# Performance work log

Hardware: AMD Instinct MI355X
Metric: run time of the kernel (lower is better)

The kernel has to match this reference:

```python
import jax, jax.numpy as jnp
import numpy as np

NUM_CLUSTERS = 5000  # labels.max()+1, fixed statically for jit
B, K, D, N = 256, 64, 2048, 50000
NHID, H2, NCLASS = 512, 256, 2


def setup_inputs() -> dict:
    key = jax.random.key(0)
    ks = jax.random.split(key, 16)
    s = lambda f_in: 1.0 / np.sqrt(f_in)
    return {
        "indexes": jax.random.randint(ks[0], (B,), 0, N),
        "features": jax.random.normal(ks[1], (N, D), dtype=jnp.float32),
        "labels": jax.random.randint(ks[2], (N,), 0, NUM_CLUSTERS),
        "domain": 1,
        "ori_0": 0,
        "ori_knn_neighbor": jax.random.randint(ks[3], (B, K), 0, N),
        "all_pred": jax.random.normal(ks[4], (B, K, NCLASS), dtype=jnp.float32),
        # GraphConv params (L-GCN style: weight [2*in, out])
        "W1": jax.random.normal(ks[5], (2 * D, NHID), jnp.float32) * s(2 * D),
        "b1": jnp.zeros((NHID,), jnp.float32),
        "W2": jax.random.normal(ks[6], (2 * NHID, H2), jnp.float32) * s(2 * NHID),
        "b2": jnp.zeros((H2,), jnp.float32),
        # classifier: Linear(256,256) -> PReLU(256) -> Linear(256,2)
        "Wc1": jax.random.normal(ks[7], (H2, H2), jnp.float32) * s(H2),
        "bc1": jnp.zeros((H2,), jnp.float32),
        "prelu_a": jnp.full((H2,), 0.25, jnp.float32),
        "Wc2": jax.random.normal(ks[8], (H2, NCLASS), jnp.float32) * s(H2),
        "bc2": jnp.zeros((NCLASS,), jnp.float32),
    }


def _gconv(x, A, W, b):
    # MeanAggregator: bmm(A, x); GraphConv: relu(cat([x, Ax]) @ W + b)
    agg = jnp.einsum('bkj,bjd->bkd', A, x)
    cat = jnp.concatenate([x, agg], axis=-1)
    return jax.nn.relu(jnp.einsum('bkd,df->bkf', cat, W) + b)


def reference(indexes, features, labels, domain, ori_0, ori_knn_neighbor, all_pred,
              W1, b1, W2, b2, Wc1, bc1, prelu_a, Wc2, bc2):
    # ---- cluster mean features (torch: index_add_ then divide; no_grad) ----
    clu_sum = jax.ops.segment_sum(features, labels, num_segments=NUM_CLUSTERS)
    nums = jax.ops.segment_sum(jnp.ones((features.shape[0],), features.dtype),
                               labels, num_segments=NUM_CLUSTERS)
    clu_mean = clu_sum / jnp.maximum(nums, 1.0)[:, None]  # [C, D]

    # ---- batched per-query subgraph construction (vectorized over B) ----
    clu_lab = labels[ori_knn_neighbor]            # [B, K]
    clu_feat = clu_mean[clu_lab]                  # [B, K, D]
    clu_feat = clu_feat.at[:, 0, :].set(features[indexes])  # pivot = raw feature

    A = jnp.einsum('bkd,bjd->bkj', clu_feat, clu_feat)       # pairwise similarity
    A = A * jnp.exp(all_pred[:, :, 1])[:, None, :]           # confidence weighting
    A = jax.nn.softmax(A, axis=-1)                           # row-normalized adjacency

    x = clu_feat / jnp.linalg.norm(clu_feat, axis=-1, keepdims=True)
    x = x - x[:, 0:1, :]                                     # center on pivot

    # (entire construction above is under torch.no_grad)
    x = jax.lax.stop_gradient(x)
    A = jax.lax.stop_gradient(A)

    # ---- GCN layers + classifier ----
    x = _gconv(x, A, W1, b1)      # [B, K, 512]
    x = _gconv(x, A, W2, b2)      # [B, K, 256]
    x0 = x.reshape(-1, H2)        # [B*K, 256]
    h = x0 @ Wc1 + bc1
    h = jnp.where(h >= 0, h, prelu_a * h)  # PReLU(256)
    logits = h @ Wc2 + bc2                 # [B*K, 2]

    # output_feat=True branch
    simm = jnp.sum(clu_mean * clu_mean, axis=1)                   # [C]
    pred = jax.nn.softmax(logits.reshape(B, K, NCLASS), axis=2)   # [B, K, 2]
    return (pred, simm)
```

## Files before the change

kernel.cpp:

```cpp
#include <hip/hip_runtime.h>
#include <math.h>

#define Bq 256
#define Kn 64
#define Dd 2048
#define Nn 50000
#define Cc 5000
#define NHID 512
#define H2d 256
#define LDH 264
#define MP 5376
#define PIVROW 5120

typedef __attribute__((ext_vector_type(8))) __bf16 bf16x8;
typedef __attribute__((ext_vector_type(4))) float f32x4;

__device__ __forceinline__ unsigned short f2bf(float f) {
    union { float f; unsigned int u; } v;
    v.f = f;
    unsigned int u = v.u;
    unsigned int r = (u + 0x7fff + ((u >> 16) & 1)) >> 16;
    return (unsigned short)r;
}
__device__ __forceinline__ float bf2f(unsigned short h) {
    union { unsigned int u; float f; } v;
    v.u = ((unsigned int)h) << 16;
    return v.f;
}


__global__ void k_zero_int(int* __restrict__ p, int n) {
    int i = blockIdx.x * 256 + threadIdx.x;
    if (i < n) p[i] = 0;
}

__global__ void k_count(const int* __restrict__ labels, int* __restrict__ cnt, int n) {
    int i = blockIdx.x * 256 + threadIdx.x;
    if (i < n) atomicAdd(&cnt[labels[i]], 1);
}

__global__ __launch_bounds__(1024) void k_scan(const int* __restrict__ cnt,
                                               int* __restrict__ off,
                                               int* __restrict__ pos, int C) {
    __shared__ int s[1024];
    __shared__ int carry;
    int tid = threadIdx.x;
    if (tid == 0) carry = 0;
    __syncthreads();
    for (int base = 0; base < C; base += 1024) {
        int i = base + tid;
        int v = (i < C) ? cnt[i] : 0;
        s[tid] = v;
        __syncthreads();
        for (int o = 1; o < 1024; o <<= 1) {
            int t = (tid >= o) ? s[tid - o] : 0;
            __syncthreads();
            s[tid] += t;
            __syncthreads();
        }
        int excl = carry + s[tid] - v;
        if (i < C) { off[i] = excl; pos[i] = excl; }
        __syncthreads();
        if (tid == 0) carry += s[1023];
        __syncthreads();
    }
}

__global__ void k_scatter(const int* __restrict__ labels, int* __restrict__ pos,
                          int* __restrict__ rowidx, int n) {
    int i = blockIdx.x * 256 + threadIdx.x;
    if (i < n) {
        int p = atomicAdd(&pos[labels[i]], 1);
        rowidx[p] = i;
    }
}

__global__ __launch_bounds__(256) void k_meansimm(
    const float* __restrict__ feat, const int* __restrict__ rowidx,
    const int* __restrict__ off, const int* __restrict__ cnt,
    float* __restrict__ clu_mean, float* __restrict__ simm,
    unsigned short* __restrict__ cn) {
    int c = blockIdx.x;
    int t = threadIdx.x;
    int n = cnt[c], st = off[c];
    float4 a0 = {0.f, 0.f, 0.f, 0.f}, a1 = {0.f, 0.f, 0.f, 0.f};
    for (int r = 0; r < n; r++) {
        const float* row = feat + (size_t)rowidx[st + r] * Dd;
        float4 v0 = *(const float4*)(row + t * 4);
        float4 v1 = *(const float4*)(row + 1024 + t * 4);
        a0.x += v0.x; a0.y += v0.y; a0.z += v0.z; a0.w += v0.w;
        a1.x += v1.x; a1.y += v1.y; a1.z += v1.z; a1.w += v1.w;
    }
    float sc = 1.f / (float)(n > 1 ? n : 1);
    a0.x *= sc; a0.y *= sc; a0.z *= sc; a0.w *= sc;
    a1.x *= sc; a1.y *= sc; a1.z *= sc; a1.w *= sc;
    float* outr = clu_mean + (size_t)c * Dd;
    *(float4*)(outr + t * 4) = a0;
    *(float4*)(outr + 1024 + t * 4) = a1;
    float ss = a0.x * a0.x + a0.y * a0.y + a0.z * a0.z + a0.w * a0.w +
               a1.x * a1.x + a1.y * a1.y + a1.z * a1.z + a1.w * a1.w;
    __shared__ float red[256];
    red[t] = ss;
    __syncthreads();
    for (int s2 = 128; s2 > 0; s2 >>= 1) {
        if (t < s2) red[t] += red[t + s2];
        __syncthreads();
    }
    if (t == 0) simm[c] = red[0];
    float tot = red[0];
    float rnn = (tot > 0.f) ? rsqrtf(tot) : 0.f;
    ushort4 c0, c1;
    c0.x = f2bf(a0.x * rnn); c0.y = f2bf(a0.y * rnn);
    c0.z = f2bf(a0.z * rnn); c0.w = f2bf(a0.w * rnn);
    c1.x = f2bf(a1.x * rnn); c1.y = f2bf(a1.y * rnn);
    c1.z = f2bf(a1.z * rnn); c1.w = f2bf(a1.w * rnn);
    unsigned short* cr = cn + (size_t)c * Dd;
    *(ushort4*)(cr + t * 4) = c0;
    *(ushort4*)(cr + 1024 + t * 4) = c1;
}

__global__ __launch_bounds__(256) void k_pivots(
    const float* __restrict__ feat, const int* __restrict__ indexes,
    unsigned short* __restrict__ PA) {
    int b = blockIdx.x, t = threadIdx.x;
    const float* row = feat + (size_t)indexes[b] * Dd;
    float4 v0 = *(const float4*)(row + t * 4);
    float4 v1 = *(const float4*)(row + 1024 + t * 4);
    float ss = v0.x * v0.x + v0.y * v0.y + v0.z * v0.z + v0.w * v0.w +
               v1.x * v1.x + v1.y * v1.y + v1.z * v1.z + v1.w * v1.w;
    __shared__ float red[256];
    red[t] = ss;
    __syncthreads();
    for (int s2 = 128; s2 > 0; s2 >>= 1) {
        if (t < s2) red[t] += red[t + s2];
        __syncthreads();
    }
    float tot = red[0];
    float rnn = (tot > 0.f) ? rsqrtf(tot) : 0.f;
    ushort4 c0, c1;
    c0.x = f2bf(v0.x * rnn); c0.y = f2bf(v0.y * rnn);
    c0.z = f2bf(v0.z * rnn); c0.w = f2bf(v0.w * rnn);
    c1.x = f2bf(v1.x * rnn); c1.y = f2bf(v1.y * rnn);
    c1.z = f2bf(v1.z * rnn); c1.w = f2bf(v1.w * rnn);
    unsigned short* cr = PA + (size_t)(PIVROW + b) * Dd;
    *(ushort4*)(cr + t * 4) = c0;
    *(ushort4*)(cr + 1024 + t * 4) = c1;
}

__global__ __launch_bounds__(256) void k_build_ax(
    const float* __restrict__ feat, const float* __restrict__ clu_mean,
    const int* __restrict__ labels, const int* __restrict__ indexes,
    const int* __restrict__ knn, const float* __restrict__ all_pred,
    float* __restrict__ Abuf) {
    __shared__ unsigned short Hs[64 * LDH];
    __shared__ unsigned short Ls[64 * LDH];
    __shared__ float Gs[64 * 65];
    __shared__ const float* rowp[64];
    __shared__ float wj64[64];

    int b = blockIdx.x, tid = threadIdx.x;
    int wave = tid >> 6, lane = tid & 63, quad = lane >> 4, l16 = lane & 15;

    if (tid < 64) {
        const float* p = (tid == 0) ? feat + (size_t)indexes[b] * Dd
                                    : clu_mean + (size_t)labels[knn[b * 64 + tid]] * Dd;
        rowp[tid] = p;
        wj64[tid] = expf(all_pred[(b * 64 + tid) * 2 + 1]);
    }
    __syncthreads();

    f32x4 acc[4];
#pragma unroll
    for (int j = 0; j < 4; j++) acc[j] = (f32x4){0.f, 0.f, 0.f, 0.f};

    for (int ch = 0; ch < 8; ch++) {
        int d0 = ch * 256;
        __syncthreads();
#pragma unroll
        for (int q = 0; q < 16; q++) {
            int e4 = tid + q * 256;
            int row = e4 >> 6;
            int c4 = (e4 & 63) * 4;
            float4 v = *(const float4*)(rowp[row] + d0 + c4);
            ushort4 h, l;
            h.x = f2bf(v.x); l.x = f2bf(v.x - bf2f(h.x));
            h.y = f2bf(v.y); l.y = f2bf(v.y - bf2f(h.y));
            h.z = f2bf(v.z); l.z = f2bf(v.z - bf2f(h.z));
            h.w = f2bf(v.w); l.w = f2bf(v.w - bf2f(h.w));
            *(ushort4*)&Hs[row * LDH + c4] = h;
            *(ushort4*)&Ls[row * LDH + c4] = l;
        }
        __syncthreads();
#pragma unroll
        for (int ks = 0; ks < 8; ks++) {
            int kk = ks * 32 + quad * 8;
            bf16x8 ah = *(const bf16x8*)&Hs[(wave * 16 + l16) * LDH + kk];
            bf16x8 al = *(const bf16x8*)&Ls[(wave * 16 + l16) * LDH + kk];
#pragma unroll
            for (int j = 0; j < 4; j++) {
                bf16x8 bh = *(const bf16x8*)&Hs[(j * 16 + l16) * LDH + kk];
                bf16x8 bl = *(const bf16x8*)&Ls[(j * 16 + l16) * LDH + kk];
                acc[j] = __builtin_amdgcn_mfma_f32_16x16x32_bf16(ah, bh, acc[j], 0, 0, 0);
                acc[j] = __builtin_amdgcn_mfma_f32_16x16x32_bf16(ah, bl, acc[j], 0, 0, 0);
                acc[j] = __builtin_amdgcn_mfma_f32_16x16x32_bf16(al, bh, acc[j], 0, 0, 0);
            }
        }
    }
    __syncthreads();
#pragma unroll
    for (int j = 0; j < 4; j++)
#pragma unroll
        for (int r = 0; r < 4; r++)
            Gs[(wave * 16 + quad * 4 + r) * 65 + j * 16 + l16] = acc[j][r];
    __syncthreads();
    if (tid < 64) {
        int r = tid;
        float mx = -1e30f;
        for (int c = 0; c < 64; c++) {
            float v = Gs[r * 65 + c] * wj64[c];
            mx = fmaxf(mx, v);
        }
        float s = 0.f;
        for (int c = 0; c < 64; c++) {
            float e = expf(Gs[r * 65 + c] * wj64[c] - mx);
            Gs[r * 65 + c] = e;
            s += e;
        }
        float inv = 1.f / s;
        float* Arow = Abuf + ((size_t)b * 64 + r) * 64;
        for (int c = 0; c < 64; c++) Arow[c] = Gs[r * 65 + c] * inv;
    }
}

template <int SPLIT>
__global__ __launch_bounds__(256) void k_pack_w(const float* __restrict__ W,
                                                unsigned short* __restrict__ Bp,
                                                int K, int Nhalf) {
    int Ntot = SPLIT ? 2 * Nhalf : Nhalf;
    int idx = blockIdx.x * 256 + threadIdx.x;
    int kb = idx / Ntot;
    int n = idx - kb * Ntot;
    ushort4 lo, hi;
    float v[8];
#pragma unroll
    for (int j = 0; j < 8; j++) {
        int k = kb * 8 + j;
        if (SPLIT)
            v[j] = (n < Nhalf) ? W[(size_t)k * Nhalf + n]
                               : W[(size_t)(K + k) * Nhalf + (n - Nhalf)];
        else
            v[j] = W[(size_t)k * Nhalf + n];
    }
    lo.x = f2bf(v[0]); lo.y = f2bf(v[1]); lo.z = f2bf(v[2]); lo.w = f2bf(v[3]);
    hi.x = f2bf(v[4]); hi.y = f2bf(v[5]); hi.z = f2bf(v[6]); hi.w = f2bf(v[7]);
    *(ushort4*)&Bp[(size_t)idx * 8] = lo;
    *(ushort4*)&Bp[(size_t)idx * 8 + 4] = hi;
}

template <int EPI>
__global__ __launch_bounds__(256) void gemm_bf16_mfma(
    const unsigned short* __restrict__ A, const unsigned short* __restrict__ Bp,
    float* __restrict__ C, int M, int K, int N,
    const float* __restrict__ bias, const float* __restrict__ pre_a) {
    __shared__ unsigned short Asm[128 * 32];
    __shared__ unsigned short Bsm[4 * 128 * 8];
    int tid = threadIdx.x;
    int wave = tid >> 6, lane = tid & 63;
    int quad = lane >> 4, l16 = lane & 15;
    int m0 = blockIdx.y * 128, n0 = blockIdx.x * 128;
    int wm = (wave >> 1) * 64, wn = (wave & 1) * 64;

    f32x4 acc[4][4];
#pragma unroll
    for (int i = 0; i < 4; i++)
#pragma unroll
        for (int j = 0; j < 4; j++) acc[i][j] = (f32x4){0.f, 0.f, 0.f, 0.f};

    int ia0 = wave * 2, ia1 = wave * 2 + 1;
    const unsigned short* gA0 = A + (size_t)(m0 + ia0 * 16 + (lane >> 2)) * K + (lane & 3) * 8;
    const unsigned short* gA1 = gA0 + (size_t)16 * K;
    const unsigned short* gB0 = Bp + (size_t)(n0 + lane) * 8 + (size_t)wave * N * 8;

    for (int k0 = 0; k0 < K; k0 += 32) {
        __syncthreads();
        size_t bko = (size_t)(k0 >> 3) * N * 8;
        __builtin_amdgcn_global_load_lds(
            (const __attribute__((address_space(1))) void*)(gA0 + k0),
            (__attribute__((address_space(3))) void*)(Asm + ia0 * 512), 16, 0, 0);
        __builtin_amdgcn_global_load_lds(
            (const __attribute__((address_space(1))) void*)(gA1 + k0),
            (__attribute__((address_space(3))) void*)(Asm + ia1 * 512), 16, 0, 0);
        __builtin_amdgcn_global_load_lds(
            (const __attribute__((address_space(1))) void*)(gB0 + bko),
            (__attribute__((address_space(3))) void*)(Bsm + wave * 1024), 16, 0, 0);
        __builtin_amdgcn_global_load_lds(
            (const __attribute__((address_space(1))) void*)(gB0 + bko + 512),
            (__attribute__((address_space(3))) void*)(Bsm + wave * 1024 + 512), 16, 0, 0);
        __syncthreads();

        bf16x8 a[4], b[4];
#pragma unroll
        for (int i = 0; i < 4; i++)
            a[i] = *(const bf16x8*)&Asm[(wm + i * 16 + l16) * 32 + quad * 8];
#pragma unroll
        for (int j = 0; j < 4; j++)
            b[j] = *(const bf16x8*)&Bsm[quad * 1024 + (wn + j * 16 + l16) * 8];
#pragma unroll
        for (int i = 0; i < 4; i++)
#pragma unroll
            for (int j = 0; j < 4; j++)
                acc[i][j] = __builtin_amdgcn_mfma_f32_16x16x32_bf16(
                    a[i], b[j], acc[i][j], 0, 0, 0);
    }

#pragma unroll
    for (int i = 0; i < 4; i++) {
#pragma unroll
        for (int j = 0; j < 4; j++) {
            int col = n0 + wn + j * 16 + l16;
            float bcol = (EPI == 1) ? bias[col] : 0.f;
            float acol = (EPI == 1) ? pre_a[col] : 0.f;
#pragma unroll
            for (int r = 0; r < 4; r++) {
                int row = m0 + wm + i * 16 + quad * 4 + r;
                float v = acc[i][j][r];
                if (EPI == 1) {
                    v += bcol;
                    v = (v >= 0.f) ? v : acol * v;
                }
                C[(size_t)row * N + col] = v;
            }
        }
    }
}

__global__ __launch_bounds__(256) void k_layer_agg1(
    const float* __restrict__ P, const float* __restrict__ Abuf,
    const int* __restrict__ labels, const int* __restrict__ knn,
    const float* __restrict__ bias, unsigned short* __restrict__ outp) {
    int b = blockIdx.x;
    int tid = threadIdx.x;
    __shared__ float Ast[64 * 68];
    __shared__ float Us[64 * 68];
    __shared__ int rowid[64];
    int ty = tid >> 4, tx = tid & 15;
    if (tid < 64)
        rowid[tid] = (tid == 0) ? (PIVROW + b) : labels[knn[b * 64 + tid]];
    const float* Ab = Abuf + (size_t)b * 64 * 64;
    for (int e4 = tid; e4 < 1024; e4 += 256) {
        float4 v = *(const float4*)(Ab + e4 * 4);
        int row = e4 >> 4;
        int c4 = (e4 & 15) * 4;
        Ast[(c4 + 0) * 68 + row] = v.x;
        Ast[(c4 + 1) * 68 + row] = v.y;
        Ast[(c4 + 2) * 68 + row] = v.z;
        Ast[(c4 + 3) * 68 + row] = v.w;
    }
    const float* Q = P + (size_t)(PIVROW + b) * 1024;
    for (int n0 = 0; n0 < NHID; n0 += 64) {
        __syncthreads();
#pragma unroll
        for (int kq = 0; kq < 4; kq++) {
            int e4 = tid + kq * 256;
            int row = e4 >> 4;
            int c4 = (e4 & 15) * 4;
            float4 v = *(const float4*)(P + (size_t)rowid[row] * 1024 + NHID + n0 + c4);
            float4 q = *(const float4*)(Q + NHID + n0 + c4);
            v.x -= q.x; v.y -= q.y; v.z -= q.z; v.w -= q.w;
            *(float4*)&Us[row * 68 + c4] = v;
        }
        __syncthreads();
        float acc[4][4];
#pragma unroll
        for (int i = 0; i < 4; i++)
#pragma unroll
            for (int j = 0; j < 4; j++) acc[i][j] = 0.f;
        for (int kk = 0; kk < 64; kk++) {
            float4 a4 = *(const float4*)&Ast[kk * 68 + ty * 4];
            float4 b4 = *(const float4*)&Us[kk * 68 + tx * 4];
            float aa[4] = {a4.x, a4.y, a4.z, a4.w};
            float bb[4] = {b4.x, b4.y, b4.z, b4.w};
#pragma unroll
            for (int i = 0; i < 4; i++)
#pragma unroll
                for (int j = 0; j < 4; j++) acc[i][j] += aa[i] * bb[j];
        }
#pragma unroll
        for (int i = 0; i < 4; i++) {
            int krow = ty * 4 + i;
            int m = b * 64 + krow;
            int n = n0 + tx * 4;
            float4 ua = *(const float4*)(P + (size_t)rowid[krow] * 1024 + n);
            float4 qa = *(const float4*)(Q + n);
            float v0 = fmaxf(ua.x - qa.x + acc[i][0] + bias[n + 0], 0.f);
            float v1 = fmaxf(ua.y - qa.y + acc[i][1] + bias[n + 1], 0.f);
            float v2 = fmaxf(ua.z - qa.z + acc[i][2] + bias[n + 2], 0.f);
            float v3 = fmaxf(ua.w - qa.w + acc[i][3] + bias[n + 3], 0.f);
            ushort4 o_;
            o_.x = f2bf(v0); o_.y = f2bf(v1); o_.z = f2bf(v2); o_.w = f2bf(v3);
            *(ushort4*)(outp + (size_t)m * NHID + n) = o_;
        }
        __syncthreads();
    }
}

template <int OBF>
__global__ __launch_bounds__(256) void k_layer_agg(
    const float* __restrict__ Uab, const float* __restrict__ Abuf,
    const float* __restrict__ bias, void* __restrict__ outp, int Nc) {
    int b = blockIdx.x;
    int tid = threadIdx.x;
    __shared__ float Ast[64 * 68];
    __shared__ float Us[64 * 68];
    int ty = tid >> 4, tx = tid & 15;
    const float* Ab = Abuf + (size_t)b * 64 * 64;
    for (int e4 = tid; e4 < 1024; e4 += 256) {
        float4 v = *(const float4*)(Ab + e4 * 4);
        int row = e4 >> 4;
        int c4 = (e4 & 15) * 4;
        Ast[(c4 + 0) * 68 + row] = v.x;
        Ast[(c4 + 1) * 68 + row] = v.y;
        Ast[(c4 + 2) * 68 + row] = v.z;
        Ast[(c4 + 3) * 68 + row] = v.w;
    }
    int ldU = 2 * Nc;
    const float* Ua = Uab;
    const float* Ub = Uab + Nc;
    for (int n0 = 0; n0 < Nc; n0 += 64) {
        __syncthreads();
#pragma unroll
        for (int kq = 0; kq < 4; kq++) {
            int e4 = tid + kq * 256;
            int row = e4 >> 4;
            int c4 = (e4 & 15) * 4;
            float4 v = *(const float4*)(Ub + (size_t)(b * 64 + row) * ldU + n0 + c4);
            *(float4*)&Us[row * 68 + c4] = v;
        }
        __syncthreads();
        float acc[4][4];
#pragma unroll
        for (int i = 0; i < 4; i++)
#pragma unroll
            for (int j = 0; j < 4; j++) acc[i][j] = 0.f;
        for (int kk = 0; kk < 64; kk++) {
            float4 a4 = *(const float4*)&Ast[kk * 68 + ty * 4];
            float4 b4 = *(const float4*)&Us[kk * 68 + tx * 4];
            float aa[4] = {a4.x, a4.y, a4.z, a4.w};
            float bb[4] = {b4.x, b4.y, b4.z, b4.w};
#pragma unroll
            for (int i = 0; i < 4; i++)
#pragma unroll
                for (int j = 0; j < 4; j++) acc[i][j] += aa[i] * bb[j];
        }
#pragma unroll
        for (int i = 0; i < 4; i++) {
            int m = b * 64 + ty * 4 + i;
            int n = n0 + tx * 4;
            float4 ua = *(const float4*)(Ua + (size_t)m * ldU + n);
            float v0 = fmaxf(ua.x + acc[i][0] + bias[n + 0], 0.f);
            float v1 = fmaxf(ua.y + acc[i][1] + bias[n + 1], 0.f);
            float v2 = fmaxf(ua.z + acc[i][2] + bias[n + 2], 0.f);
            float v3 = fmaxf(ua.w + acc[i][3] + bias[n + 3], 0.f);
            if (OBF) {
                ushort4 o_;
                o_.x = f2bf(v0); o_.y = f2bf(v1); o_.z = f2bf(v2); o_.w = f2bf(v3);
                *(ushort4*)((unsigned short*)outp + (size_t)m * Nc + n) = o_;
            } else {
                float4 o_ = {v0, v1, v2, v3};
                *(float4*)((float*)outp + (size_t)m * Nc + n) = o_;
            }
        }
        __syncthreads();
    }
}

__global__ __launch_bounds__(256) void k_logits(
    const float* __restrict__ h, const float* __restrict__ Wc2,
    const float* __restrict__ bc2, float* __restrict__ pred) {
    __shared__ float p0[256], p1[256];
    int tid = threadIdx.x;
    int r = tid >> 2, s = tid & 3;
    int m = blockIdx.x * 64 + r;
    const float* hr = h + (size_t)m * 256;
    float l0 = 0.f, l1 = 0.f;
    for (int k = s; k < 256; k += 4) {
        float hv = hr[k];
        l0 += hv * Wc2[2 * k];
        l1 += hv * Wc2[2 * k + 1];
    }
    p0[tid] = l0;
    p1[tid] = l1;
    __syncthreads();
    if (s == 0) {
        float L0 = p0[tid] + p0[tid + 1] + p0[tid + 2] + p0[tid + 3] + bc2[0];
        float L1 = p1[tid] + p1[tid + 1] + p1[tid + 2] + p1[tid + 3] + bc2[1];
        float mx = fmaxf(L0, L1);
        float e0 = expf(L0 - mx), e1 = expf(L1 - mx);
        float inv = 1.f / (e0 + e1);
        pred[2 * m] = e0 * inv;
        pred[2 * m + 1] = e1 * inv;
    }
}

extern "C" void kernel_launch(void* const* d_in, const int* in_sizes, int n_in,
                              void* d_out, int out_size, void* d_ws, size_t ws_size,
                              hipStream_t stream) {
    const int* indexes = (const int*)d_in[0];
    const float* features = (const float*)d_in[1];
    const int* labels = (const int*)d_in[2];
    const int* knn = (const int*)d_in[5];
    const float* all_pred = (const float*)d_in[6];
    const float* W1 = (const float*)d_in[7];
    const float* b1 = (const float*)d_in[8];
    const float* W2 = (const float*)d_in[9];
    const float* b2 = (const float*)d_in[10];
    const float* Wc1 = (const float*)d_in[11];
    const float* bc1 = (const float*)d_in[12];
    const float* pre_a = (const float*)d_in[13];
    const float* Wc2 = (const float*)d_in[14];
    const float* bc2 = (const float*)d_in[15];
    float* out = (float*)d_out;

    char* w = (char*)d_ws;
    size_t o = 0;
    auto carve = [&](size_t bytes) -> char* {
        char* p = w + o;
        o += (bytes + 255) & ~(size_t)255;
        return p;
    };
    int* cnt = (int*)carve((size_t)Cc * 4);
    int* off = (int*)carve((size_t)Cc * 4);
    int* pos = (int*)carve((size_t)Cc * 4);
    int* rowidx = (int*)carve((size_t)Nn * 4);
    float* clu_mean = (float*)carve((size_t)Cc * Dd * 4);
    unsigned short* PA = (unsigned short*)carve((size_t)MP * Dd * 2);
    float* Pout = (float*)carve((size_t)MP * 2 * NHID * 4);
    float* Abuf = (float*)carve((size_t)Bq * Kn * Kn * 4);
    unsigned short* Bp1 = (unsigned short*)carve((size_t)(Dd / 8) * 1024 * 8 * 2);
    unsigned short* x1 = (unsigned short*)carve((size_t)Bq * Kn * NHID * 2);
    float* V = (float*)carve((size_t)Bq * Kn * 2 * H2d * 4);
    unsigned short* Bp2 = (unsigned short*)carve((size_t)(NHID / 8) * 512 * 8 * 2);
    unsigned short* x2 = (unsigned short*)carve((size_t)Bq * Kn * H2d * 2);
    float* h = (float*)carve((size_t)Bq * Kn * H2d * 4);
    unsigned short* Bpc = (unsigned short*)carve((size_t)(H2d / 8) * 256 * 8 * 2);

    float* simm_out = out + (size_t)Bq * Kn * 2;

    k_zero_int<<<(Cc + 255) / 256, 256, 0, stream>>>(cnt, Cc);
    k_count<<<(Nn + 255) / 256, 256, 0, stream>>>(labels, cnt, Nn);
    k_scan<<<1, 1024, 0, stream>>>(cnt, off, pos, Cc);
    k_scatter<<<(Nn + 255) / 256, 256, 0, stream>>>(labels, pos, rowidx, Nn);

    {
        int npad = (PIVROW - Cc) * Dd / 2;
        k_zero_int<<<(npad + 255) / 256, 256, 0, stream>>>(
            (int*)(PA + (size_t)Cc * Dd), npad);
    }

    k_meansimm<<<Cc, 256, 0, stream>>>(features, rowidx, off, cnt, clu_mean,
                                       simm_out, PA);

    k_pivots<<<Bq, 256, 0, stream>>>(features, indexes, PA);

    k_build_ax<<<Bq, 256, 0, stream>>>(features, clu_mean, labels, indexes, knn,
                                       all_pred, Abuf);

    k_pack_w<1><<<(Dd / 8) * 1024 / 256, 256, 0, stream>>>(W1, Bp1, Dd, NHID);
    k_pack_w<1><<<(NHID / 8) * 512 / 256, 256, 0, stream>>>(W2, Bp2, NHID, H2d);
    k_pack_w<0><<<(H2d / 8) * 256 / 256, 256, 0, stream>>>(Wc1, Bpc, H2d, H2d);

    {
        dim3 g(1024 / 128, MP / 128);
        gemm_bf16_mfma<0><<<g, 256, 0, stream>>>(PA, Bp1, Pout, MP, Dd, 1024,
                                                 nullptr, nullptr);
    }
    k_layer_agg1<<<Bq, 256, 0, stream>>>(Pout, Abuf, labels, knn, b1, x1);

    {
        dim3 g(512 / 128, (Bq * Kn) / 128);
        gemm_bf16_mfma<0><<<g, 256, 0, stream>>>(x1, Bp2, V, Bq * Kn, NHID, 512,
                                                 nullptr, nullptr);
    }
    k_layer_agg<1><<<Bq, 256, 0, stream>>>(V, Abuf, b2, x2, H2d);

    {
        dim3 g(256 / 128, (Bq * Kn) / 128);
        gemm_bf16_mfma<1><<<g, 256, 0, stream>>>(x2, Bpc, h, Bq * Kn, H2d, 256,
                                                 bc1, pre_a);
    }
    k_logits<<<(Bq * Kn) / 64, 256, 0, stream>>>(h, Wc2, bc2, out);

    (void)in_sizes; (void)n_in; (void)out_size; (void)ws_size;
}
```

Measured before the change: 837.4 us.

## Fuse launches, premix layer-2 aggregation before GEMM, fold classifier into GEMM epilogue

Merges the zeroing, pivot normalisation and weight-packing kernels into fewer launches, and replaces the single-block scan with an atomic offset allocator. Layer 2 now aggregates x1 with A before the GEMM (A·x then one K=1024 GEMM with a bias+ReLU epilogue) instead of computing a 2x-wide output and aggregating after it. The classifier's second linear layer is folded into the first GEMM's epilogue through shuffle reductions and atomics, which removes the fp32 h buffer. Layer-1 aggregation is split across two blocks per query. The atomic allocator makes cluster order nondeterministic, and float atomics make the logit sums order-dependent.

```diff
diff --git a/kernel.cpp b/kernel.cpp
--- a/kernel.cpp
+++ b/kernel.cpp
@@ -28,10 +28,18 @@
     return v.f;
 }
 
-
-__global__ void k_zero_int(int* __restrict__ p, int n) {
+__global__ void k_zero_multi(int* __restrict__ p0, int n0,
+                             int* __restrict__ p1, int n1,
+                             int* __restrict__ p2, int n2,
+                             int* __restrict__ p3, int n3) {
     int i = blockIdx.x * 256 + threadIdx.x;
-    if (i < n) p[i] = 0;
+    if (i < n0) { p0[i] = 0; return; }
+    i -= n0;
+    if (i < n1) { p1[i] = 0; return; }
+    i -= n1;
+    if (i < n2) { p2[i] = 0; return; }
+    i -= n2;
+    if (i < n3) p3[i] = 0;
 }
 
 __global__ void k_count(const int* __restrict__ labels, int* __restrict__ cnt, int n) {
@@ -39,30 +47,13 @@
     if (i < n) atomicAdd(&cnt[labels[i]], 1);
 }
 
-__global__ __launch_bounds__(1024) void k_scan(const int* __restrict__ cnt,
-                                               int* __restrict__ off,
-                                               int* __restrict__ pos, int C) {
-    __shared__ int s[1024];
-    __shared__ int carry;
-    int tid = threadIdx.x;
-    if (tid == 0) carry = 0;
-    __syncthreads();
-    for (int base = 0; base < C; base += 1024) {
-        int i = base + tid;
-        int v = (i < C) ? cnt[i] : 0;
-        s[tid] = v;
-        __syncthreads();
-        for (int o = 1; o < 1024; o <<= 1) {
-            int t = (tid >= o) ? s[tid - o] : 0;
-            __syncthreads();
-            s[tid] += t;
-            __syncthreads();
-        }
-        int excl = carry + s[tid] - v;
-        if (i < C) { off[i] = excl; pos[i] = excl; }
-        __syncthreads();
-        if (tid == 0) carry += s[1023];
-        __syncthreads();
+__global__ void k_alloc(const int* __restrict__ cnt, int* __restrict__ off,
+                        int* __restrict__ pos, int* __restrict__ total, int C) {
+    int c = blockIdx.x * 256 + threadIdx.x;
+    if (c < C) {
+        int o = atomicAdd(total, cnt[c]);
+        off[c] = o;
+        pos[c] = o;
     }
 }
 
@@ -78,10 +69,39 @@
 __global__ __launch_bounds__(256) void k_meansimm(
     const float* __restrict__ feat, const int* __restrict__ rowidx,
     const int* __restrict__ off, const int* __restrict__ cnt,
+    const int* __restrict__ indexes,
     float* __restrict__ clu_mean, float* __restrict__ simm,
-    unsigned short* __restrict__ cn) {
+    unsigned short* __restrict__ PA) {
     int c = blockIdx.x;
     int t = threadIdx.x;
+    __shared__ float red[256];
+
+    if (c >= Cc) {
+        int b = c - Cc;
+        const float* row = feat + (size_t)indexes[b] * Dd;
+        float4 v0 = *(const float4*)(row + t * 4);
+        float4 v1 = *(const float4*)(row + 1024 + t * 4);
+        float ss = v0.x * v0.x + v0.y * v0.y + v0.z * v0.z + v0.w * v0.w +
+                   v1.x * v1.x + v1.y * v1.y + v1.z * v1.z + v1.w * v1.w;
+        red[t] = ss;
+        __syncthreads();
+        for (int s2 = 128; s2 > 0; s2 >>= 1) {
+            if (t < s2) red[t] += red[t + s2];
+            __syncthreads();
+        }
+        float tot = red[0];
+        float rnn = (tot > 0.f) ? rsqrtf(tot) : 0.f;
+        ushort4 c0, c1;
+        c0.x = f2bf(v0.x * rnn); c0.y = f2bf(v0.y * rnn);
+        c0.z = f2bf(v0.z * rnn); c0.w = f2bf(v0.w * rnn);
+        c1.x = f2bf(v1.x * rnn); c1.y = f2bf(v1.y * rnn);
+        c1.z = f2bf(v1.z * rnn); c1.w = f2bf(v1.w * rnn);
+        unsigned short* cr = PA + (size_t)(PIVROW + b) * Dd;
+        *(ushort4*)(cr + t * 4) = c0;
+        *(ushort4*)(cr + 1024 + t * 4) = c1;
+        return;
+    }
+
     int n = cnt[c], st = off[c];
     float4 a0 = {0.f, 0.f, 0.f, 0.f}, a1 = {0.f, 0.f, 0.f, 0.f};
     for (int r = 0; r < n; r++) {
@@ -99,7 +119,6 @@
     *(float4*)(outr + 1024 + t * 4) = a1;
     float ss = a0.x * a0.x + a0.y * a0.y + a0.z * a0.z + a0.w * a0.w +
                a1.x * a1.x + a1.y * a1.y + a1.z * a1.z + a1.w * a1.w;
-    __shared__ float red[256];
     red[t] = ss;
     __syncthreads();
     for (int s2 = 128; s2 > 0; s2 >>= 1) {
@@ -114,35 +133,7 @@
     c0.z = f2bf(a0.z * rnn); c0.w = f2bf(a0.w * rnn);
     c1.x = f2bf(a1.x * rnn); c1.y = f2bf(a1.y * rnn);
     c1.z = f2bf(a1.z * rnn); c1.w = f2bf(a1.w * rnn);
-    unsigned short* cr = cn + (size_t)c * Dd;
-    *(ushort4*)(cr + t * 4) = c0;
-    *(ushort4*)(cr + 1024 + t * 4) = c1;
-}
-
-__global__ __launch_bounds__(256) void k_pivots(
-    const float* __restrict__ feat, const int* __restrict__ indexes,
-    unsigned short* __restrict__ PA) {
-    int b = blockIdx.x, t = threadIdx.x;
-    const float* row = feat + (size_t)indexes[b] * Dd;
-    float4 v0 = *(const float4*)(row + t * 4);
-    float4 v1 = *(const float4*)(row + 1024 + t * 4);
-    float ss = v0.x * v0.x + v0.y * v0.y + v0.z * v0.z + v0.w * v0.w +
-               v1.x * v1.x + v1.y * v1.y + v1.z * v1.z + v1.w * v1.w;
-    __shared__ float red[256];
-    red[t] = ss;
-    __syncthreads();
-    for (int s2 = 128; s2 > 0; s2 >>= 1) {
-        if (t < s2) red[t] += red[t + s2];
-        __syncthreads();
-    }
-    float tot = red[0];
-    float rnn = (tot > 0.f) ? rsqrtf(tot) : 0.f;
-    ushort4 c0, c1;
-    c0.x = f2bf(v0.x * rnn); c0.y = f2bf(v0.y * rnn);
-    c0.z = f2bf(v0.z * rnn); c0.w = f2bf(v0.w * rnn);
-    c1.x = f2bf(v1.x * rnn); c1.y = f2bf(v1.y * rnn);
-    c1.z = f2bf(v1.z * rnn); c1.w = f2bf(v1.w * rnn);
-    unsigned short* cr = PA + (size_t)(PIVROW + b) * Dd;
+    unsigned short* cr = PA + (size_t)c * Dd;
     *(ushort4*)(cr + t * 4) = c0;
     *(ushort4*)(cr + 1024 + t * 4) = c1;
 }
@@ -232,36 +223,50 @@
     }
 }
 
-template <int SPLIT>
-__global__ __launch_bounds__(256) void k_pack_w(const float* __restrict__ W,
-                                                unsigned short* __restrict__ Bp,
-                                                int K, int Nhalf) {
-    int Ntot = SPLIT ? 2 * Nhalf : Nhalf;
-    int idx = blockIdx.x * 256 + threadIdx.x;
+__device__ __forceinline__ void pack_item(const float* __restrict__ W,
+                                          unsigned short* __restrict__ Bp,
+                                          int K, int Nhalf, int split, int idx) {
+    int Ntot = split ? 2 * Nhalf : Nhalf;
     int kb = idx / Ntot;
     int n = idx - kb * Ntot;
-    ushort4 lo, hi;
     float v[8];
 #pragma unroll
     for (int j = 0; j < 8; j++) {
         int k = kb * 8 + j;
-        if (SPLIT)
+        if (split)
             v[j] = (n < Nhalf) ? W[(size_t)k * Nhalf + n]
                                : W[(size_t)(K + k) * Nhalf + (n - Nhalf)];
         else
             v[j] = W[(size_t)k * Nhalf + n];
     }
+    ushort4 lo, hi;
     lo.x = f2bf(v[0]); lo.y = f2bf(v[1]); lo.z = f2bf(v[2]); lo.w = f2bf(v[3]);
     hi.x = f2bf(v[4]); hi.y = f2bf(v[5]); hi.z = f2bf(v[6]); hi.w = f2bf(v[7]);
     *(ushort4*)&Bp[(size_t)idx * 8] = lo;
     *(ushort4*)&Bp[(size_t)idx * 8 + 4] = hi;
 }
 
+__global__ __launch_bounds__(256) void k_pack_all(
+    const float* __restrict__ W1, const float* __restrict__ W2,
+    const float* __restrict__ Wc1, unsigned short* __restrict__ Bp1,
+    unsigned short* __restrict__ Bp2, unsigned short* __restrict__ Bpc) {
+    int blk = blockIdx.x;
+    int tid = threadIdx.x;
+    if (blk < 1024) {
+        pack_item(W1, Bp1, Dd, NHID, 1, blk * 256 + tid);
+    } else if (blk < 1024 + 128) {
+        pack_item(W2, Bp2, 2 * NHID, H2d, 0, (blk - 1024) * 256 + tid);
+    } else {
+        pack_item(Wc1, Bpc, H2d, H2d, 0, (blk - 1152) * 256 + tid);
+    }
+}
+
 template <int EPI>
 __global__ __launch_bounds__(256) void gemm_bf16_mfma(
     const unsigned short* __restrict__ A, const unsigned short* __restrict__ Bp,
-    float* __restrict__ C, int M, int K, int N,
-    const float* __restrict__ bias, const float* __restrict__ pre_a) {
+    void* __restrict__ Cout, int M, int K, int N,
+    const float* __restrict__ bias, const float* __restrict__ pre_a,
+    const float* __restrict__ wc2, float* __restrict__ lbuf) {
     __shared__ unsigned short Asm[128 * 32];
     __shared__ unsigned short Bsm[4 * 128 * 8];
     int tid = threadIdx.x;
@@ -313,22 +318,59 @@
                     a[i], b[j], acc[i][j], 0, 0, 0);
     }
 
-#pragma unroll
-    for (int i = 0; i < 4; i++) {
-#pragma unroll
-        for (int j = 0; j < 4; j++) {
-            int col = n0 + wn + j * 16 + l16;
-            float bcol = (EPI == 1) ? bias[col] : 0.f;
-            float acol = (EPI == 1) ? pre_a[col] : 0.f;
+    if (EPI == 0) {
+        float* C = (float*)Cout;
+#pragma unroll
+        for (int i = 0; i < 4; i++)
+#pragma unroll
+            for (int j = 0; j < 4; j++) {
+                int col = n0 + wn + j * 16 + l16;
+#pragma unroll
+                for (int r = 0; r < 4; r++) {
+                    int row = m0 + wm + i * 16 + quad * 4 + r;
+                    C[(size_t)row * N + col] = acc[i][j][r];
+                }
+            }
+    } else if (EPI == 2) {
+        unsigned short* C = (unsigned short*)Cout;
+#pragma unroll
+        for (int i = 0; i < 4; i++)
+#pragma unroll
+            for (int j = 0; j < 4; j++) {
+                int col = n0 + wn + j * 16 + l16;
+                float bcol = bias[col];
+#pragma unroll
+                for (int r = 0; r < 4; r++) {
+                    int row = m0 + wm + i * 16 + quad * 4 + r;
+                    float v = acc[i][j][r] + bcol;
+                    v = fmaxf(v, 0.f);
+                    C[(size_t)row * N + col] = f2bf(v);
+                }
+            }
+    } else {
+#pragma unroll
+        for (int i = 0; i < 4; i++) {
 #pragma unroll
             for (int r = 0; r < 4; r++) {
-                int row = m0 + wm + i * 16 + quad * 4 + r;
-                float v = acc[i][j][r];
-                if (EPI == 1) {
-                    v += bcol;
-                    v = (v >= 0.f) ? v : acol * v;
+                float l0 = 0.f, l1 = 0.f;
+#pragma unroll
+                for (int j = 0; j < 4; j++) {
+                    int col = n0 + wn + j * 16 + l16;
+                    float v = acc[i][j][r] + bias[col];
+                    v = (v >= 0.f) ? v : pre_a[col] * v;
+                    l0 += v * wc2[2 * col];
+                    l1 += v * wc2[2 * col + 1];
                 }
-                C[(size_t)row * N + col] = v;
+#pragma unroll
+                for (int mm = 1; mm < 16; mm <<= 1) {
+                    l0 += __shfl_xor(l0, mm, 64);
+                    l1 += __shfl_xor(l1, mm, 64);
+                }
+                if (l16 == 0) {
+                    int row = m0 + wm + i * 16 + quad * 4 + r;
+                    atomicAdd(&lbuf[2 * row], l0);
+                    atomicAdd(&lbuf[2 * row + 1], l1);
+                }
             }
         }
     }
@@ -339,6 +381,7 @@
     const int* __restrict__ labels, const int* __restrict__ knn,
     const float* __restrict__ bias, unsigned short* __restrict__ outp) {
     int b = blockIdx.x;
+    int half = blockIdx.y;
     int tid = threadIdx.x;
     __shared__ float Ast[64 * 68];
     __shared__ float Us[64 * 68];
@@ -357,7 +400,7 @@
         Ast[(c4 + 3) * 68 + row] = v.w;
     }
     const float* Q = P + (size_t)(PIVROW + b) * 1024;
-    for (int n0 = 0; n0 < NHID; n0 += 64) {
+    for (int n0 = half * (NHID / 2); n0 < (half + 1) * (NHID / 2); n0 += 64) {
         __syncthreads();
 #pragma unroll
         for (int kq = 0; kq < 4; kq++) {
@@ -398,17 +441,17 @@
             float v3 = fmaxf(ua.w - qa.w + acc[i][3] + bias[n + 3], 0.f);
             ushort4 o_;
             o_.x = f2bf(v0); o_.y = f2bf(v1); o_.z = f2bf(v2); o_.w = f2bf(v3);
-            *(ushort4*)(outp + (size_t)m * NHID + n) = o_;
-        }
-        __syncthreads();
-    }
-}
-
-template <int OBF>
-__global__ __launch_bounds__(256) void k_layer_agg(
-    const float* __restrict__ Uab, const float* __restrict__ Abuf,
-    const float* __restrict__ bias, void* __restrict__ outp, int Nc) {
+            *(ushort4*)(outp + (size_t)m * 1024 + n) = o_;
+        }
+        __syncthreads();
+    }
+}
+
+__global__ __launch_bounds__(256) void k_premix(
+    const unsigned short* __restrict__ xy1, const float* __restrict__ Abuf,
+    unsigned short* __restrict__ yout) {
     int b = blockIdx.x;
+    int half = blockIdx.y;
     int tid = threadIdx.x;
     __shared__ float Ast[64 * 68];
     __shared__ float Us[64 * 68];
@@ -423,18 +466,18 @@
         Ast[(c4 + 2) * 68 + row] = v.z;
         Ast[(c4 + 3) * 68 + row] = v.w;
     }
-    int ldU = 2 * Nc;
-    const float* Ua = Uab;
-    const float* Ub = Uab + Nc;
-    for (int n0 = 0; n0 < Nc; n0 += 64) {
+    for (int n0 = half * (NHID / 2); n0 < (half + 1) * (NHID / 2); n0 += 64) {
         __syncthreads();
 #pragma unroll
         for (int kq = 0; kq < 4; kq++) {
             int e4 = tid + kq * 256;
             int row = e4 >> 4;
             int c4 = (e4 & 15) * 4;
-            float4 v = *(const float4*)(Ub + (size_t)(b * 64 + row) * ldU + n0 + c4);
-            *(float4*)&Us[row * 68 + c4] = v;
+            ushort4 u = *(const ushort4*)(xy1 + (size_t)(b * 64 + row) * 1024 + n0 + c4);
+            Us[row * 68 + c4 + 0] = bf2f(u.x);
+            Us[row * 68 + c4 + 1] = bf2f(u.y);
+            Us[row * 68 + c4 + 2] = bf2f(u.z);
+            Us[row * 68 + c4 + 3] = bf2f(u.w);
         }
         __syncthreads();
         float acc[4][4];
@@ -456,44 +499,23 @@
         for (int i = 0; i < 4; i++) {
             int m = b * 64 + ty * 4 + i;
             int n = n0 + tx * 4;
-            float4 ua = *(const float4*)(Ua + (size_t)m * ldU + n);
-            float v0 = fmaxf(ua.x + acc[i][0] + bias[n + 0], 0.f);
-            float v1 = fmaxf(ua.y + acc[i][1] + bias[n + 1], 0.f);
-            float v2 = fmaxf(ua.z + acc[i][2] + bias[n + 2], 0.f);
-            float v3 = fmaxf(ua.w + acc[i][3] + bias[n + 3], 0.f);
-            if (OBF) {
-                ushort4 o_;
-                o_.x = f2bf(v0); o_.y = f2bf(v1); o_.z = f2bf(v2); o_.w = f2bf(v3);
-                *(ushort4*)((unsigned short*)outp + (size_t)m * Nc + n) = o_;
-            } else {
-                float4 o_ = {v0, v1, v2, v3};
-                *(float4*)((float*)outp + (size_t)m * Nc + n) = o_;
-            }
-        }
-        __syncthreads();
-    }
-}
-
-__global__ __launch_bounds__(256) void k_logits(
-    const float* __restrict__ h, const float* __restrict__ Wc2,
-    const float* __restrict__ bc2, float* __restrict__ pred) {
-    __shared__ float p0[256], p1[256];
-    int tid = threadIdx.x;
-    int r = tid >> 2, s = tid & 3;
-    int m = blockIdx.x * 64 + r;
-    const float* hr = h + (size_t)m * 256;
-    float l0 = 0.f, l1 = 0.f;
-    for (int k = s; k < 256; k += 4) {
-        float hv = hr[k];
-        l0 += hv * Wc2[2 * k];
-        l1 += hv * Wc2[2 * k + 1];
-    }
-    p0[tid] = l0;
-    p1[tid] = l1;
-    __syncthreads();
-    if (s == 0) {
-        float L0 = p0[tid] + p0[tid + 1] + p0[tid + 2] + p0[tid + 3] + bc2[0];
-        float L1 = p1[tid] + p1[tid + 1] + p1[tid + 2] + p1[tid + 3] + bc2[1];
+            ushort4 o_;
+            o_.x = f2bf(acc[i][0]);
+            o_.y = f2bf(acc[i][1]);
+            o_.z = f2bf(acc[i][2]);
+            o_.w = f2bf(acc[i][3]);
+            *(ushort4*)(yout + (size_t)m * 1024 + 512 + n) = o_;
+        }
+        __syncthreads();
+    }
+}
+
+__global__ void k_soft2(const float* __restrict__ lbuf, const float* __restrict__ bc2,
+                        float* __restrict__ pred) {
+    int m = blockIdx.x * 256 + threadIdx.x;
+    if (m < Bq * Kn) {
+        float L0 = lbuf[2 * m] + bc2[0];
+        float L1 = lbuf[2 * m + 1] + bc2[1];
         float mx = fmaxf(L0, L1);
         float e0 = expf(L0 - mx), e1 = expf(L1 - mx);
         float inv = 1.f / (e0 + e1);
@@ -531,64 +553,64 @@
     int* cnt = (int*)carve((size_t)Cc * 4);
     int* off = (int*)carve((size_t)Cc * 4);
     int* pos = (int*)carve((size_t)Cc * 4);
+    int* total = (int*)carve(4);
     int* rowidx = (int*)carve((size_t)Nn * 4);
     float* clu_mean = (float*)carve((size_t)Cc * Dd * 4);
     unsigned short* PA = (unsigned short*)carve((size_t)MP * Dd * 2);
     float* Pout = (float*)carve((size_t)MP * 2 * NHID * 4);
     float* Abuf = (float*)carve((size_t)Bq * Kn * Kn * 4);
     unsigned short* Bp1 = (unsigned short*)carve((size_t)(Dd / 8) * 1024 * 8 * 2);
-    unsigned short* x1 = (unsigned short*)carve((size_t)Bq * Kn * NHID * 2);
-    float* V = (float*)carve((size_t)Bq * Kn * 2 * H2d * 4);
-    unsigned short* Bp2 = (unsigned short*)carve((size_t)(NHID / 8) * 512 * 8 * 2);
+    unsigned short* xy1 = (unsigned short*)carve((size_t)Bq * Kn * 1024 * 2);
+    unsigned short* Bp2 = (unsigned short*)carve((size_t)(2 * NHID / 8) * H2d * 8 * 2);
     unsigned short* x2 = (unsigned short*)carve((size_t)Bq * Kn * H2d * 2);
-    float* h = (float*)carve((size_t)Bq * Kn * H2d * 4);
     unsigned short* Bpc = (unsigned short*)carve((size_t)(H2d / 8) * 256 * 8 * 2);
+    float* lbuf = (float*)carve((size_t)Bq * Kn * 2 * 4);
 
     float* simm_out = out + (size_t)Bq * Kn * 2;
 
-    k_zero_int<<<(Cc + 255) / 256, 256, 0, stream>>>(cnt, Cc);
+    {
+        int nPad = (PIVROW - Cc) * Dd / 2;
+        int nLb = Bq * Kn * 2;
+        int ntot = Cc + nPad + nLb + 1;
+        k_zero_multi<<<(ntot + 255) / 256, 256, 0, stream>>>(
+            cnt, Cc, (int*)(PA + (size_t)Cc * Dd), nPad, (int*)lbuf, nLb, total, 1);
+    }
     k_count<<<(Nn + 255) / 256, 256, 0, stream>>>(labels, cnt, Nn);
-    k_scan<<<1, 1024, 0, stream>>>(cnt, off, pos, Cc);
+    k_alloc<<<(Cc + 255) / 256, 256, 0, stream>>>(cnt, off, pos, total, Cc);
     k_scatter<<<(Nn + 255) / 256, 256, 0, stream>>>(labels, pos, rowidx, Nn);
 
-    {
-        int npad = (PIVROW - Cc) * Dd / 2;
-        k_zero_int<<<(npad + 255) / 256, 256, 0, stream>>>(
-            (int*)(PA + (size_t)Cc * Dd), npad);
-    }
-
-    k_meansimm<<<Cc, 256, 0, stream>>>(features, rowidx, off, cnt, clu_mean,
-                                       simm_out, PA);
-
-    k_pivots<<<Bq, 256, 0, stream>>>(features, indexes, PA);
+    k_meansimm<<<Cc + Bq, 256, 0, stream>>>(features, rowidx, off, cnt, indexes,
+                                            clu_mean, simm_out, PA);
 
     k_build_ax<<<Bq, 256, 0, stream>>>(features, clu_mean, labels, indexes, knn,
                                        all_pred, Abuf);
 
-    k_pack_w<1><<<(Dd / 8) * 1024 / 256, 256, 0, stream>>>(W1, Bp1, Dd, NHID);
-    k_pack_w<1><<<(NHID / 8) * 512 / 256, 256, 0, stream>>>(W2, Bp2, NHID, H2d);
-    k_pack_w<0><<<(H2d / 8) * 256 / 256, 256, 0, stream>>>(Wc1, Bpc, H2d, H2d);
+    k_pack_all<<<1184, 256, 0, stream>>>(W1, W2, Wc1, Bp1, Bp2, Bpc);
 
     {
         dim3 g(1024 / 128, MP / 128);
         gemm_bf16_mfma<0><<<g, 256, 0, stream>>>(PA, Bp1, Pout, MP, Dd, 1024,
-                                                 nullptr, nullptr);
-    }
-    k_layer_agg1<<<Bq, 256, 0, stream>>>(Pout, Abuf, labels, knn, b1, x1);
-
+                                                 nullptr, nullptr, nullptr, nullptr);
+    }
     {
-        dim3 g(512 / 128, (Bq * Kn) / 128);
-        gemm_bf16_mfma<0><<<g, 256, 0, stream>>>(x1, Bp2, V, Bq * Kn, NHID, 512,
-                                                 nullptr, nullptr);
-    }
-    k_layer_agg<1><<<Bq, 256, 0, stream>>>(V, Abuf, b2, x2, H2d);
-
+        dim3 g(Bq, 2);
+        k_layer_agg1<<<g, 256, 0, stream>>>(Pout, Abuf, labels, knn, b1, xy1);
+    }
     {
-        dim3 g(256 / 128, (Bq * Kn) / 128);
-        gemm_bf16_mfma<1><<<g, 256, 0, stream>>>(x2, Bpc, h, Bq * Kn, H2d, 256,
-                                                 bc1, pre_a);
-    }
-    k_logits<<<(Bq * Kn) / 64, 256, 0, stream>>>(h, Wc2, bc2, out);
+        dim3 g(Bq, 2);
+        k_premix<<<g, 256, 0, stream>>>(xy1, Abuf, xy1);
+    }
+    {
+        dim3 g(H2d / 128, (Bq * Kn) / 128);
+        gemm_bf16_mfma<2><<<g, 256, 0, stream>>>(xy1, Bp2, x2, Bq * Kn, 1024, H2d,
+                                                 b2, nullptr, nullptr, nullptr);
+    }
+    {
+        dim3 g(H2d / 128, (Bq * Kn) / 128);
+        gemm_bf16_mfma<3><<<g, 256, 0, stream>>>(x2, Bpc, nullptr, Bq * Kn, H2d, H2d,
+                                                 bc1, pre_a, Wc2, lbuf);
+    }
+    k_soft2<<<(Bq * Kn + 255) / 256, 256, 0, stream>>>(lbuf, bc2, out);
 
     (void)in_sizes; (void)n_in; (void)out_size; (void)ws_size;
 }
```

Measured after the change: 829.7 us. Within noise of the previous version (-0.9%).
